# Optimization experiments

Measured on AMD Instinct MI355X. Metric: run time of the kernel, lower is better.

Reference implementation:

```python
import jax, jax.numpy as jnp
import numpy as np

NUM_PROJS = 7
BLOCK = 256       # HyperAttention block_size
SAMPLE = 256      # HyperAttention sample_size
NUM_HEADS = 16

def _hamming_perm(n):
    a = np.array([0, 1])
    for _ in range(n - 1):
        a = np.concatenate([a, a[::-1] + a.max() + 1])
    return a

_PERM = jnp.asarray(_hamming_perm(NUM_PROJS))           # [128] gray-code-ish bucket reorder
_ENC = (2 ** jnp.arange(NUM_PROJS)).astype(jnp.int32)   # [7]

def _lsh_hash(mat, proj_dir):
    # mat: [B,H,N,d], proj_dir: [d,7] -> bucket ids [B,H,N]
    bits = jnp.einsum('bhnd,dr->bhnr', mat, proj_dir) > 0
    ids = (bits * _ENC).sum(-1)
    return _PERM[ids]

def _attn_lse(q, k, v, scale, bias=None):
    s = jnp.einsum('...qd,...kd->...qk', q, k) * scale
    if bias is not None:
        s = s + bias
    lse = jax.nn.logsumexp(s, axis=-1, keepdims=True)
    o = jnp.einsum('...qk,...kd->...qd', jnp.exp(s - lse), v)
    return o, lse

def _gather(t, idx):
    # gather rows along axis 2: out[b,h,s] = t[b,h,idx[b,h,s]]
    return jnp.take_along_axis(t, idx[..., None], axis=2)

def setup_inputs():
    key = jax.random.key(0)
    ks = jax.random.split(key, 7)
    B, L, D, INNER = 2, 8192, 1024, 1024
    x = jax.random.normal(ks[0], (B, L, D), jnp.float32)
    W_qkv = jax.random.normal(ks[1], (D, 3 * INNER), jnp.float32) / np.sqrt(D)
    b_qkv = jnp.zeros((3 * INNER,), jnp.float32)
    W_proj = jax.random.normal(ks[2], (INNER, D), jnp.float32) / np.sqrt(INNER)
    b_proj = jnp.zeros((D,), jnp.float32)
    proj_dir = jax.random.normal(ks[3], (INNER // NUM_HEADS, NUM_PROJS), jnp.float32)
    sampled_set = jax.random.randint(ks[4], (B, NUM_HEADS, SAMPLE), 0, L)
    return {"x": x, "W_qkv": W_qkv, "b_qkv": b_qkv, "W_proj": W_proj,
            "b_proj": b_proj, "proj_dir": proj_dir, "sampled_set": sampled_set}

def reference(x, W_qkv, b_qkv, W_proj, b_proj, proj_dir, sampled_set):
    B, L, D = x.shape
    qkv = (x @ W_qkv + b_qkv).reshape(B, L, 3, NUM_HEADS, -1).transpose(2, 0, 3, 1, 4)
    q, k, v = qkv[0], qkv[1], qkv[2]                      # [B,H,L,dh]
    dh = q.shape[-1]
    scale = dh ** -0.5
    # 1. sortLSH: stable sort q and k rows by angular-LSH bucket id
    q_idx = jnp.argsort(_lsh_hash(q, proj_dir), axis=2, stable=True)
    k_idx = jnp.argsort(_lsh_hash(k, proj_dir), axis=2, stable=True)
    q_idx_inv = jnp.argsort(q_idx, axis=2, stable=True)   # to restore row order
    qs = _gather(q, q_idx)
    ksort = _gather(k, k_idx)
    vsort = _gather(v, k_idx)
    # block-diagonal exact attention over the sorted order (L % BLOCK == 0 here)
    nb = L // BLOCK
    ab, lb = _attn_lse(qs.reshape(B, NUM_HEADS, nb, BLOCK, dh),
                       ksort.reshape(B, NUM_HEADS, nb, BLOCK, dh),
                       vsort.reshape(B, NUM_HEADS, nb, BLOCK, dh), scale)
    attn_block = ab.reshape(B, NUM_HEADS, L, dh)
    lse_block = lb.reshape(B, NUM_HEADS, L, 1)
    # 2. residual uniformly-sampled attention, masking entries already covered by blocks
    k_sub = _gather(ksort, sampled_set)                   # [B,H,SAMPLE,dh]
    v_sub = _gather(vsort, sampled_set)
    blk_q = jnp.arange(L)[None, None, :, None] // BLOCK   # query block id (query_block_size==BLOCK)
    mask = blk_q == (sampled_set // BLOCK)[:, :, None, :]  # [B,H,L,SAMPLE]
    bias = jnp.where(mask, jnp.finfo(x.dtype).min, 0.0).astype(x.dtype)
    attn_res, lse_res = _attn_lse(qs, k_sub, v_sub, scale, bias)
    lse_res = lse_res + jnp.log(jnp.float32(L) / SAMPLE)  # importance weight n_key/sample_size
    # combine the two attentions via their log-sum-exps
    c = 1.0 / (1.0 + jnp.exp(lse_res - lse_block))
    attn = c * attn_block + (1.0 - c) * attn_res
    out = _gather(attn, q_idx_inv)                        # un-sort rows back to input order
    out = out.transpose(0, 2, 1, 3).reshape(B, L, -1)     # [B,L,inner]
    return out @ W_proj + b_proj
```

## Files before the change

### kernel.cpp

```cpp
#include <hip/hip_runtime.h>
#include <hip/hip_fp16.h>
#include <math.h>


typedef _Float16 f16x8 __attribute__((ext_vector_type(8)));
typedef _Float16 f16x4 __attribute__((ext_vector_type(4)));
typedef __fp16 fp16x2 __attribute__((ext_vector_type(2)));
typedef float f32x4 __attribute__((ext_vector_type(4)));

#define WLIST_CAP 524288
#define TAU 0.06f

__device__ __forceinline__ void gl_lds16(const void* g, void* s) {
    __builtin_amdgcn_global_load_lds(
        (const __attribute__((address_space(1))) unsigned int*)g,
        (__attribute__((address_space(3))) unsigned int*)s, 16, 0, 0);
}

__global__ __launch_bounds__(256) void fold_kernel(
    const float* __restrict__ W, const float* __restrict__ bias,
    const float* __restrict__ proj, double* __restrict__ fold,
    double* __restrict__ bfold, _Float16* __restrict__ foldh,
    float* __restrict__ bfold32)
{
    int idx = blockIdx.x * 256 + threadIdx.x;
    if (idx < 2 * 16 * 7 * 1024) {
        int task = idx / 7168;
        int rem = idx - task * 7168;
        int i = rem / 7;
        int r = rem - i * 7;
        int h = task & 15, w = task >> 4;
        double s = 0.0;
        const float* wp = W + (size_t)i * 3072 + w * 1024 + h * 64;
        for (int d = 0; d < 64; ++d)
            s += (double)wp[d] * (double)proj[d * 7 + r];
        fold[idx] = s;
        foldh[((size_t)task * 7 + r) * 1024 + i] = (_Float16)s;
    }
    if (idx < 32768)
        foldh[229376 + idx] = (_Float16)0.f;
    if (idx < 224) {
        int r = idx % 7;
        int task = idx / 7;
        int h = task & 15, w = task >> 4;
        double s = 0.0;
        for (int d = 0; d < 64; ++d)
            s += (double)bias[w * 1024 + h * 64 + d] * (double)proj[d * 7 + r];
        bfold[idx] = s;
        bfold32[idx] = (float)s;
    }
}

__global__ __launch_bounds__(256) void hashext_kernel(
    const float* __restrict__ scores, const float* __restrict__ bfold32,
    int* __restrict__ hq, int* __restrict__ hk,
    int* __restrict__ wcount, int* __restrict__ wlist)
{
    int tid = blockIdx.x * 256 + threadIdx.x;
    int row = tid >> 5, task = tid & 31;
    const float* sp = scores + (size_t)row * 256 + task * 7;
    int id = 0, fl = 0;
#pragma unroll
    for (int r = 0; r < 7; ++r) {
        float val = sp[r] + bfold32[task * 7 + r];
        if (fabsf(val) < TAU) fl = 1;
        if (val > 0.f) id |= (1 << r);
    }
    int hsh = id ^ (id >> 1);
    int w = task >> 4, h = task & 15;
    int b = row >> 13, l = row & 8191;
    (w ? hk : hq)[((size_t)(b * 16 + h) << 13) + l] = hsh;
    if (fl) {
        int slot = atomicAdd(wcount, 1);
        if (slot < WLIST_CAP) wlist[slot] = task * 16384 + row;
    }
}

__global__ __launch_bounds__(256) void refine_kernel(
    const float* __restrict__ x, const double* __restrict__ fold,
    const double* __restrict__ bfold, const int* __restrict__ wcount,
    const int* __restrict__ wlist, int* __restrict__ hq, int* __restrict__ hk)
{
    int n = *wcount;
    if (n > WLIST_CAP) n = WLIST_CAP;
    int lane = threadIdx.x & 63;
    int wid = (blockIdx.x * 256 + threadIdx.x) >> 6;
    int nw = gridDim.x * 4;
    for (int e = wid; e < n; e += nw) {
        int code = wlist[e];
        int task = code >> 14, grow = code & 16383;
        const double* f = fold + (size_t)task * 7168;
        const float* xp = x + (size_t)grow * 1024;
        double acc[7] = {0, 0, 0, 0, 0, 0, 0};
        for (int i = lane; i < 1024; i += 64) {
            double xv = (double)xp[i];
#pragma unroll
            for (int rr = 0; rr < 7; ++rr)
                acc[rr] = fma(xv, f[(size_t)i * 7 + rr], acc[rr]);
        }
        int id = 0;
#pragma unroll
        for (int rr = 0; rr < 7; ++rr) {
            double a = acc[rr];
#pragma unroll
            for (int off = 32; off > 0; off >>= 1) a += __shfl_xor(a, off, 64);
            if (a + bfold[task * 7 + rr] > 0.0) id |= (1 << rr);
        }
        if (lane == 0) {
            int hsh = id ^ (id >> 1);
            int w = task >> 4, h = task & 15;
            int b = grow >> 13, l = grow & 8191;
            (w ? hk : hq)[((size_t)(b * 16 + h) << 13) + l] = hsh;
        }
    }
}

__global__ __launch_bounds__(256) void sort_kernel(
    const int* __restrict__ hq, const int* __restrict__ hk,
    int* __restrict__ qidx, int* __restrict__ kidx,
    int* __restrict__ qrank, int* __restrict__ krank)
{
    __shared__ unsigned short cnt[128][128];
    __shared__ int tot[128];
    __shared__ int base[128];
    int blk = blockIdx.x;
    int sel = blk >> 5, bh = blk & 31;
    const int* hp = (sel ? hk : hq) + ((size_t)bh << 13);
    int* op = (sel ? kidx : qidx) + ((size_t)bh << 13);
    int* rp = (sel ? krank : qrank) + ((size_t)bh << 13);
    int t = threadIdx.x;
    for (int i = t; i < 128 * 128 / 2; i += 256) ((unsigned int*)cnt)[i] = 0u;
    __syncthreads();
    if (t < 128) {
        const int* p = hp + t * 64;
        for (int j = 0; j < 64; ++j) cnt[t][p[j]]++;
    }
    __syncthreads();
    if (t < 128) {
        int run = 0;
        for (int c = 0; c < 128; ++c) {
            int x2 = cnt[c][t];
            cnt[c][t] = (unsigned short)run;
            run += x2;
        }
        tot[t] = run;
    }
    __syncthreads();
    if (t == 0) {
        int run = 0;
        for (int v = 0; v < 128; ++v) { base[v] = run; run += tot[v]; }
    }
    __syncthreads();
    if (t < 128) {
        const int* p = hp + t * 64;
        for (int j = 0; j < 64; ++j) {
            int v = p[j];
            int c = cnt[t][v];
            cnt[t][v] = (unsigned short)(c + 1);
            int pos = base[v] + c;
            op[pos] = t * 64 + j;
            rp[t * 64 + j] = pos;
        }
    }
}

__global__ __launch_bounds__(256) void castx_kernel(
    const float* __restrict__ x, _Float16* __restrict__ xh)
{
    int i = blockIdx.x * 256 + threadIdx.x;
    float4 f = ((const float4*)x)[i];
    _Float16 h4[4] = {(_Float16)f.x, (_Float16)f.y, (_Float16)f.z, (_Float16)f.w};
    *(short4*)&xh[(size_t)i * 4] = *(short4*)h4;
}

__global__ __launch_bounds__(256) void transpose_kernel(
    const float* __restrict__ W, _Float16* __restrict__ Wt, int K, int N)
{
    __shared__ float tile[32][33];
    int bx = blockIdx.x, by = blockIdx.y;
    int tx = threadIdx.x & 31, ty = threadIdx.x >> 5;
    for (int i = ty; i < 32; i += 8)
        tile[i][tx] = W[(size_t)(by * 32 + i) * N + bx * 32 + tx];
    __syncthreads();
    for (int i = ty; i < 32; i += 8)
        Wt[(size_t)(bx * 32 + i) * K + by * 32 + tx] = (_Float16)tile[tx][i];
}

__global__ __launch_bounds__(256) void gather_samp_kernel(
    const _Float16* __restrict__ ks, const _Float16* __restrict__ vs,
    const int* __restrict__ sampled, _Float16* __restrict__ ksamp,
    _Float16* __restrict__ vsamp)
{
    int bh = blockIdx.x;
    int key = blockIdx.y * 64 + (threadIdx.x >> 2);
    int qtr = (threadIdx.x & 3) * 16;
    size_t hb = (size_t)bh << 13;
    int p = sampled[bh * 256 + key];
    size_t src = (hb + p) * 64 + qtr;
    size_t dst = ((size_t)bh * 256 + key) * 64 + qtr;
    *(f16x8*)(ksamp + dst)     = *(const f16x8*)(ks + src);
    *(f16x8*)(ksamp + dst + 8) = *(const f16x8*)(ks + src + 8);
    *(f16x8*)(vsamp + dst)     = *(const f16x8*)(vs + src);
    *(f16x8*)(vsamp + dst + 8) = *(const f16x8*)(vs + src + 8);
}

template <int MODE>
__global__ __launch_bounds__(256) void mfma_gemm(
    const _Float16* __restrict__ A, const _Float16* __restrict__ Bt,
    const float* __restrict__ bias, float* __restrict__ C, int K, int N)
{
    __shared__ __align__(16) _Float16 As[128 * 64];
    __shared__ __align__(16) _Float16 Bs[128 * 64];
    int t = threadIdx.x;
    int w = t >> 6, l = t & 63;
    int m0 = blockIdx.y * 128, n0 = blockIdx.x * 128;
    int srow = 32 * w + (l >> 3);
    int sslot = ((l & 7) ^ (l >> 3)) * 8;
    const _Float16* ga = A + (size_t)(m0 + srow) * K + sslot;
    const _Float16* gb = Bt + (size_t)(n0 + srow) * K + sslot;
    int wr = w >> 1, wc = w & 1;
    int rl = l & 15, ks = l >> 4;
    f32x4 acc[4][4];
#pragma unroll
    for (int m = 0; m < 4; ++m)
#pragma unroll
        for (int n = 0; n < 4; ++n) acc[m][n] = (f32x4){0.f, 0.f, 0.f, 0.f};
    for (int kk = 0; kk < K; kk += 64) {
        __syncthreads();
#pragma unroll
        for (int i = 0; i < 4; ++i) {
            gl_lds16(ga + (size_t)(8 * i) * K + kk, (char*)As + (32 * w + 8 * i) * 128);
            gl_lds16(gb + (size_t)(8 * i) * K + kk, (char*)Bs + (32 * w + 8 * i) * 128);
        }
        __syncthreads();
        f16x8 af[4][2], bf[4][2];
#pragma unroll
        for (int m = 0; m < 4; ++m) {
            int r = 64 * wr + 16 * m + rl;
            int sw = (r & 7) << 4;
#pragma unroll
            for (int s = 0; s < 2; ++s)
                af[m][s] = *(const f16x8*)((char*)As + r * 128 + (((s * 4 + ks) << 4) ^ sw));
        }
#pragma unroll
        for (int n = 0; n < 4; ++n) {
            int r = 64 * wc + 16 * n + rl;
            int sw = (r & 7) << 4;
#pragma unroll
            for (int s = 0; s < 2; ++s)
                bf[n][s] = *(const f16x8*)((char*)Bs + r * 128 + (((s * 4 + ks) << 4) ^ sw));
        }
#pragma unroll
        for (int m = 0; m < 4; ++m)
#pragma unroll
            for (int n = 0; n < 4; ++n) {
                acc[m][n] = __builtin_amdgcn_mfma_f32_16x16x32_f16(
                    af[m][0], bf[n][0], acc[m][n], 0, 0, 0);
                acc[m][n] = __builtin_amdgcn_mfma_f32_16x16x32_f16(
                    af[m][1], bf[n][1], acc[m][n], 0, 0, 0);
            }
    }
#pragma unroll
    for (int m = 0; m < 4; ++m)
#pragma unroll
        for (int n = 0; n < 4; ++n) {
            int gn = n0 + 64 * wc + 16 * n + rl;
            float bv = (MODE == 2) ? 0.f : bias[gn];
#pragma unroll
            for (int j = 0; j < 4; ++j) {
                int gm = m0 + 64 * wr + 16 * m + 4 * ks + j;
                C[(size_t)gm * N + gn] = acc[m][n][j] + bv;
            }
        }
}

__global__ __launch_bounds__(512) void gemm_qkv_kernel(
    const _Float16* __restrict__ Wt, const _Float16* __restrict__ xh,
    const float* __restrict__ bias, _Float16* __restrict__ Q,
    _Float16* __restrict__ Kb, _Float16* __restrict__ Vb,
    const int* __restrict__ qrank, const int* __restrict__ krank)
{
    extern __shared__ __align__(16) char smem[];
    const int K = 1024;
    int bid = blockIdx.x;
    int xcd = bid & 7, slot = bid >> 3;
    int ty = slot / 12, tx = slot - ty * 12;
    int m0 = tx * 256;
    int n0 = (xcd * 8 + ty) * 256;
    int t = threadIdx.x;
    int w = t >> 6, l = t & 63;
    int wr = w >> 2, wc = w & 3;
    int rl = l & 15, ks = l >> 4;
    int srow = t >> 3;
    int sslot = (t & 7) ^ ((t >> 3) & 7);
    const _Float16* gA = Wt + (size_t)m0 * K + sslot * 8;
    const _Float16* gB = xh + (size_t)n0 * K + sslot * 8;
    char* dstT = smem + t * 16;

    auto STAGE = [&](int buf, int op, int half, int kt) {
        const _Float16* src = op ? gB : gA;
        char* d = dstT + buf * 65536 + op * 32768 + half * 16384;
        size_t ro = (size_t)(half * 128 + srow) * K + kt * 64;
        gl_lds16(src + ro, d);
        gl_lds16(src + ro + (size_t)64 * K, d + 8192);
    };

    int fbase = m0 + 128 * wr;
    int s0 = fbase >> 10;
    int h0 = (fbase >> 6) & 15;
    int b2 = n0 >> 13;
    const int* rk = (s0 == 0) ? qrank : krank;
    _Float16* dq = (s0 == 0) ? Q : (s0 == 1 ? Kb : Vb);
    int tl = (n0 & 8191) + 64 * wc;
    int pos[2][4];
#pragma unroll
    for (int hf = 0; hf < 2; ++hf)
#pragma unroll
        for (int n = 0; n < 4; ++n)
            pos[hf][n] = rk[((size_t)(b2 * 16 + h0 + hf) << 13) + tl + 16 * n + rl];
    float4 bias4[8];
#pragma unroll
    for (int m = 0; m < 8; ++m)
        bias4[m] = *(const float4*)&bias[fbase + 16 * m + 4 * ks];

    f32x4 acc[8][4];
#pragma unroll
    for (int m = 0; m < 8; ++m)
#pragma unroll
        for (int n = 0; n < 4; ++n) acc[m][n] = (f32x4){0.f, 0.f, 0.f, 0.f};

    STAGE(0, 0, 0, 0); STAGE(0, 0, 1, 0); STAGE(0, 1, 0, 0); STAGE(0, 1, 1, 0);
    STAGE(1, 1, 0, 1); STAGE(1, 1, 1, 1);

    for (int tt = 0; tt < 16; ++tt) {
        int buf = tt & 1, obuf = buf ^ 1;
        if (tt < 15) asm volatile("s_waitcnt vmcnt(4)" ::: "memory");
        else         asm volatile("s_waitcnt vmcnt(0)" ::: "memory");
        __builtin_amdgcn_sched_barrier(0);
        __builtin_amdgcn_s_barrier();
        __builtin_amdgcn_sched_barrier(0);
        const char* Ab = smem + buf * 65536;
        const char* Bb = Ab + 32768;
        f16x8 bf[4][2], af01[2][2];
#pragma unroll
        for (int n = 0; n < 4; ++n) {
            int r = 64 * wc + 16 * n + rl;
            int sw = (r & 7) << 4;
            bf[n][0] = *(const f16x8*)(Bb + r * 128 + ((ks << 4) ^ sw));
            bf[n][1] = *(const f16x8*)(Bb + r * 128 + (((4 + ks) << 4) ^ sw));
        }
#pragma unroll
        for (int m = 0; m < 2; ++m) {
            int r = 128 * wr + 16 * m + rl;
            int sw = (r & 7) << 4;
            af01[m][0] = *(const f16x8*)(Ab + r * 128 + ((ks << 4) ^ sw));
            af01[m][1] = *(const f16x8*)(Ab + r * 128 + (((4 + ks) << 4) ^ sw));
        }
        if (tt + 1 < 16) STAGE(obuf, 0, 0, tt + 1);
        __builtin_amdgcn_s_setprio(1);
#pragma unroll
        for (int m = 0; m < 2; ++m)
#pragma unroll
            for (int n = 0; n < 4; ++n) {
                acc[m][n] = __builtin_amdgcn_mfma_f32_16x16x32_f16(
                    af01[m][0], bf[n][0], acc[m][n], 0, 0, 0);
                acc[m][n] = __builtin_amdgcn_mfma_f32_16x16x32_f16(
                    af01[m][1], bf[n][1], acc[m][n], 0, 0, 0);
            }
        __builtin_amdgcn_s_setprio(0);
        f16x8 af27[6][2];
#pragma unroll
        for (int m = 0; m < 6; ++m) {
            int r = 128 * wr + 16 * (m + 2) + rl;
            int sw = (r & 7) << 4;
            af27[m][0] = *(const f16x8*)(Ab + r * 128 + ((ks << 4) ^ sw));
            af27[m][1] = *(const f16x8*)(Ab + r * 128 + (((4 + ks) << 4) ^ sw));
        }
        if (tt + 1 < 16) STAGE(obuf, 0, 1, tt + 1);
        __builtin_amdgcn_s_setprio(1);
#pragma unroll
        for (int m = 0; m < 2; ++m)
#pragma unroll
            for (int n = 0; n < 4; ++n) {
                acc[m + 2][n] = __builtin_amdgcn_mfma_f32_16x16x32_f16(
                    af27[m][0], bf[n][0], acc[m + 2][n], 0, 0, 0);
                acc[m + 2][n] = __builtin_amdgcn_mfma_f32_16x16x32_f16(
                    af27[m][1], bf[n][1], acc[m + 2][n], 0, 0, 0);
            }
        __builtin_amdgcn_s_setprio(0);
        asm volatile("" ::: "memory");
        __builtin_amdgcn_s_barrier();
        __builtin_amdgcn_sched_barrier(0);
        if (tt + 2 < 16) STAGE(buf, 1, 0, tt + 2);
        __builtin_amdgcn_s_setprio(1);
#pragma unroll
        for (int m = 2; m < 4; ++m)
#pragma unroll
            for (int n = 0; n < 4; ++n) {
                acc[m + 2][n] = __builtin_amdgcn_mfma_f32_16x16x32_f16(
                    af27[m][0], bf[n][0], acc[m + 2][n], 0, 0, 0);
                acc[m + 2][n] = __builtin_amdgcn_mfma_f32_16x16x32_f16(
                    af27[m][1], bf[n][1], acc[m + 2][n], 0, 0, 0);
            }
        __builtin_amdgcn_s_setprio(0);
        if (tt + 2 < 16) STAGE(buf, 1, 1, tt + 2);
        __builtin_amdgcn_s_setprio(1);
#pragma unroll
        for (int m = 4; m < 6; ++m)
#pragma unroll
            for (int n = 0; n < 4; ++n) {
                acc[m + 2][n] = __builtin_amdgcn_mfma_f32_16x16x32_f16(
                    af27[m][0], bf[n][0], acc[m + 2][n], 0, 0, 0);
                acc[m + 2][n] = __builtin_amdgcn_mfma_f32_16x16x32_f16(
                    af27[m][1], bf[n][1], acc[m + 2][n], 0, 0, 0);
            }
        __builtin_amdgcn_s_setprio(0);
    }
#pragma unroll
    for (int m = 0; m < 8; ++m) {
        int hf = m >> 2;
        size_t bhb = ((size_t)(b2 * 16 + h0 + hf) << 13);
        int d = 16 * (m & 3) + 4 * ks;
#pragma unroll
        for (int n = 0; n < 4; ++n) {
            f16x4 st;
            st[0] = (_Float16)(acc[m][n][0] + bias4[m].x);
            st[1] = (_Float16)(acc[m][n][1] + bias4[m].y);
            st[2] = (_Float16)(acc[m][n][2] + bias4[m].z);
            st[3] = (_Float16)(acc[m][n][3] + bias4[m].w);
            *(f16x4*)(dq + (bhb + pos[hf][n]) * 64 + d) = st;
        }
    }
}

__global__ __launch_bounds__(256) void attn_mfma_kernel(
    const _Float16* __restrict__ qs_, const _Float16* __restrict__ ks_,
    const _Float16* __restrict__ vs_, const _Float16* __restrict__ ksamp,
    const _Float16* __restrict__ vsamp, const int* __restrict__ qidx,
    const int* __restrict__ sampled, _Float16* __restrict__ pre)
{
    __shared__ __align__(16) _Float16 Vt[2][64 * 68];
    int bid = blockIdx.x;
    int nb = (bid & 7) * 256 + (bid >> 3);
    int bh = nb >> 6, qb = (nb >> 1) & 31, half = nb & 1;
    int bb = bh >> 4, hh = bh & 15;
    size_t hb = (size_t)bh << 13;
    size_t bhs = (size_t)bh * 256;
    int t = threadIdx.x;
    int w = t >> 6, l = t & 63;
    int g = l >> 4, c16 = l & 15;
    int kg = t & 15, dg = t >> 4;
    int qw0 = qb * 256 + half * 128 + w * 32;
    const _Float16 qs = (_Float16)0.125f;

    int orig[2];
    f16x8 qf[2][2];
#pragma unroll
    for (int n = 0; n < 2; ++n) {
        int row = qw0 + 16 * n + c16;
        orig[n] = qidx[hb + row];
        const _Float16* qp = qs_ + (hb + row) * 64 + g * 8;
        qf[n][0] = *(const f16x8*)(qp);
        qf[n][1] = *(const f16x8*)(qp + 32);
#pragma unroll
        for (int j = 0; j < 8; ++j) { qf[n][0][j] *= qs; qf[n][1][j] *= qs; }
    }
    f32x4 o[4][2];
    float mr[2], lr[2];
#pragma unroll
    for (int n = 0; n < 2; ++n) {
        mr[n] = -1e30f; lr[n] = 0.f;
#pragma unroll
        for (int d2 = 0; d2 < 4; ++d2) o[d2][n] = (f32x4){0.f, 0.f, 0.f, 0.f};
    }
    const float LOG32 = 3.4657359027997265f;

    {
        const _Float16* vb = vs_ + (hb + qb * 256) * 64;
        f16x4 vr[4];
#pragma unroll
        for (int j2 = 0; j2 < 4; ++j2)
            vr[j2] = *(const f16x4*)(vb + (4 * kg + j2) * 64 + 4 * dg);
#pragma unroll
        for (int i = 0; i < 4; ++i) {
            f16x4 o4 = {vr[0][i], vr[1][i], vr[2][i], vr[3][i]};
            *(f16x4*)&Vt[0][(4 * dg + i) * 68 + 4 * kg] = o4;
        }
    }

    for (int c = 0; c < 8; ++c) {
        int cur = c & 1, nxt = cur ^ 1;
        bool samp = c >= 4;
        __syncthreads();
        const _Float16* kb = samp ? ksamp + (bhs + (size_t)(c - 4) * 64) * 64
                                  : ks_ + (hb + qb * 256 + (size_t)c * 64) * 64;
        f16x8 kf[4][2];
#pragma unroll
        for (int m = 0; m < 4; ++m) {
            const _Float16* kp = kb + (16 * m + c16) * 64 + g * 8;
            kf[m][0] = *(const f16x8*)(kp);
            kf[m][1] = *(const f16x8*)(kp + 32);
        }
        int4 spv[4];
        if (samp) {
#pragma unroll
            for (int m = 0; m < 4; ++m)
                spv[m] = *(const int4*)(sampled + bhs + (c - 4) * 64 + 16 * m + 4 * g);
        }
        f32x4 sacc[4][2];
#pragma unroll
        for (int m = 0; m < 4; ++m)
#pragma unroll
            for (int n = 0; n < 2; ++n) sacc[m][n] = (f32x4){0.f, 0.f, 0.f, 0.f};
#pragma unroll
        for (int m = 0; m < 4; ++m) {
#pragma unroll
            for (int n = 0; n < 2; ++n)
                sacc[m][n] = __builtin_amdgcn_mfma_f32_16x16x32_f16(
                    kf[m][0], qf[n][0], sacc[m][n], 0, 0, 0);
#pragma unroll
            for (int n = 0; n < 2; ++n)
                sacc[m][n] = __builtin_amdgcn_mfma_f32_16x16x32_f16(
                    kf[m][1], qf[n][1], sacc[m][n], 0, 0, 0);
        }
        f16x4 vrn[4];
        if (c < 7) {
            const _Float16* vb = (c + 1 >= 4)
                ? vsamp + (bhs + (size_t)(c - 3) * 64) * 64
                : vs_ + (hb + qb * 256 + (size_t)(c + 1) * 64) * 64;
#pragma unroll
            for (int j2 = 0; j2 < 4; ++j2)
                vrn[j2] = *(const f16x4*)(vb + (4 * kg + j2) * 64 + 4 * dg);
        }
        f16x4 av[4][4];
#pragma unroll
        for (int m = 0; m < 4; ++m)
#pragma unroll
            for (int d2 = 0; d2 < 4; ++d2)
                av[m][d2] = *(const f16x4*)&Vt[cur][(16 * d2 + c16) * 68 + 16 * m + 4 * g];
        bool msk[4][4];
#pragma unroll
        for (int m = 0; m < 4; ++m) {
            msk[m][0] = samp && ((spv[m].x >> 8) == qb);
            msk[m][1] = samp && ((spv[m].y >> 8) == qb);
            msk[m][2] = samp && ((spv[m].z >> 8) == qb);
            msk[m][3] = samp && ((spv[m].w >> 8) == qb);
        }
        float badd = samp ? LOG32 : 0.f;
#pragma unroll
        for (int n = 0; n < 2; ++n) {
            float sv[16];
#pragma unroll
            for (int m = 0; m < 4; ++m)
#pragma unroll
                for (int r = 0; r < 4; ++r)
                    sv[4 * m + r] = msk[m][r] ? -1e30f : sacc[m][n][r] + badd;
            float a0 = fmaxf(fmaxf(sv[0], sv[1]), sv[2]);
            float a1 = fmaxf(fmaxf(sv[3], sv[4]), sv[5]);
            float a2 = fmaxf(fmaxf(sv[6], sv[7]), sv[8]);
            float a3 = fmaxf(fmaxf(sv[9], sv[10]), sv[11]);
            float a4 = fmaxf(fmaxf(sv[12], sv[13]), sv[14]);
            float cm = fmaxf(fmaxf(fmaxf(a0, a1), a2), fmaxf(fmaxf(a3, a4), sv[15]));
            cm = fmaxf(cm, __shfl_xor(cm, 16, 64));
            cm = fmaxf(cm, __shfl_xor(cm, 32, 64));
            if (__any(cm > mr[n])) {
                float nm = fmaxf(mr[n], cm);
                float fq = __expf(mr[n] - nm);
                mr[n] = nm;
                lr[n] *= fq;
#pragma unroll
                for (int d2 = 0; d2 < 4; ++d2) {
                    o[d2][n][0] *= fq; o[d2][n][1] *= fq;
                    o[d2][n][2] *= fq; o[d2][n][3] *= fq;
                }
            }
            float pv16[16];
#pragma unroll
            for (int r = 0; r < 16; ++r) pv16[r] = __expf(sv[r] - mr[n]);
            float s0 = (pv16[0] + pv16[1]) + (pv16[2] + pv16[3]);
            float s1 = (pv16[4] + pv16[5]) + (pv16[6] + pv16[7]);
            float s2 = (pv16[8] + pv16[9]) + (pv16[10] + pv16[11]);
            float s3 = (pv16[12] + pv16[13]) + (pv16[14] + pv16[15]);
            float ps = (s0 + s1) + (s2 + s3);
            ps += __shfl_xor(ps, 16, 64);
            ps += __shfl_xor(ps, 32, 64);
            lr[n] += ps;
            f16x4 pb[4];
#pragma unroll
            for (int m = 0; m < 4; ++m) {
                fp16x2 c0 = __builtin_amdgcn_cvt_pkrtz(pv16[4 * m + 0], pv16[4 * m + 1]);
                fp16x2 c1 = __builtin_amdgcn_cvt_pkrtz(pv16[4 * m + 2], pv16[4 * m + 3]);
                pb[m][0] = (_Float16)c0[0]; pb[m][1] = (_Float16)c0[1];
                pb[m][2] = (_Float16)c1[0]; pb[m][3] = (_Float16)c1[1];
            }
#pragma unroll
            for (int d2 = 0; d2 < 4; ++d2)
#pragma unroll
                for (int m = 0; m < 4; ++m)
                    o[d2][n] = __builtin_amdgcn_mfma_f32_16x16x16f16(
                        av[m][d2], pb[m], o[d2][n], 0, 0, 0);
        }
        if (c < 7) {
#pragma unroll
            for (int i = 0; i < 4; ++i) {
                f16x4 o4 = {vrn[0][i], vrn[1][i], vrn[2][i], vrn[3][i]};
                *(f16x4*)&Vt[nxt][(4 * dg + i) * 68 + 4 * kg] = o4;
            }
        }
    }
#pragma unroll
    for (int n = 0; n < 2; ++n) {
        float invl = 1.f / lr[n];
        _Float16* pp = pre + ((size_t)(bb * 8192 + orig[n])) * 1024 + hh * 64;
#pragma unroll
        for (int d2 = 0; d2 < 4; ++d2) {
            f16x4 st;
            st[0] = (_Float16)(o[d2][n][0] * invl);
            st[1] = (_Float16)(o[d2][n][1] * invl);
            st[2] = (_Float16)(o[d2][n][2] * invl);
            st[3] = (_Float16)(o[d2][n][3] * invl);
            *(f16x4*)(pp + 16 * d2 + 4 * g) = st;
        }
    }
}

extern "C" void kernel_launch(void* const* d_in, const int* in_sizes, int n_in,
                              void* d_out, int out_size, void* d_ws, size_t ws_size,
                              hipStream_t stream)
{
    (void)in_sizes; (void)n_in; (void)out_size; (void)ws_size;
    const float* x     = (const float*)d_in[0];
    const float* Wqkv  = (const float*)d_in[1];
    const float* bqkv  = (const float*)d_in[2];
    const float* Wproj = (const float*)d_in[3];
    const float* bproj = (const float*)d_in[4];
    const float* proj  = (const float*)d_in[5];
    const int*   samp  = (const int*)d_in[6];
    float* out = (float*)d_out;

    char* ws = (char*)d_ws;
    size_t off = 0;
    auto take = [&](size_t bytes) {
        char* p = ws + off;
        off = (off + bytes + 255) & ~(size_t)255;
        return p;
    };
    _Float16* xh  = (_Float16*)take(33554432);
    _Float16* q   = (_Float16*)take(33554432);
    _Float16* k   = (_Float16*)take(33554432);
    _Float16* v   = (_Float16*)take(33554432);
    float* scores = (float*)take(16777216);
    _Float16* Wtq = (_Float16*)take(6291456);
    _Float16* Wtp = (_Float16*)take(2097152);
    _Float16* foldh = (_Float16*)take(524288);
    _Float16* ksamp = (_Float16*)take(1048576);
    _Float16* vsamp = (_Float16*)take(1048576);
    double* fold   = (double*)take(1835008);
    double* bfold  = (double*)take(1792);
    float* bfold32 = (float*)take(896);
    int* wcount = (int*)take(256);
    int* wlist  = (int*)take(WLIST_CAP * 4);
    int* hq    = (int*)take(1048576);
    int* hk    = (int*)take(1048576);
    int* qidx  = (int*)take(1048576);
    int* kidx  = (int*)take(1048576);
    int* qrank = (int*)take(1048576);
    int* krank = (int*)take(1048576);
    _Float16* pre = xh;

    (void)hipFuncSetAttribute((const void*)gemm_qkv_kernel,
                              hipFuncAttributeMaxDynamicSharedMemorySize, 131072);
    (void)hipMemsetAsync(wcount, 0, 4, stream);
    castx_kernel<<<dim3(16384), dim3(256), 0, stream>>>(x, xh);
    fold_kernel<<<dim3(896), dim3(256), 0, stream>>>(
        Wqkv, bqkv, proj, fold, bfold, foldh, bfold32);
    mfma_gemm<2><<<dim3(2, 128), dim3(256), 0, stream>>>(
        xh, foldh, nullptr, scores, 1024, 256);
    hashext_kernel<<<dim3(2048), dim3(256), 0, stream>>>(
        scores, bfold32, hq, hk, wcount, wlist);
    refine_kernel<<<dim3(2048), dim3(256), 0, stream>>>(
        x, fold, bfold, wcount, wlist, hq, hk);
    sort_kernel<<<dim3(64), dim3(256), 0, stream>>>(
        hq, hk, qidx, kidx, qrank, krank);
    transpose_kernel<<<dim3(96, 32), dim3(256), 0, stream>>>(Wqkv, Wtq, 1024, 3072);
    transpose_kernel<<<dim3(32, 32), dim3(256), 0, stream>>>(Wproj, Wtp, 1024, 1024);
    gemm_qkv_kernel<<<dim3(768), dim3(512), 131072, stream>>>(
        Wtq, xh, bqkv, q, k, v, qrank, krank);
    gather_samp_kernel<<<dim3(32, 4), dim3(256), 0, stream>>>(
        k, v, samp, ksamp, vsamp);
    attn_mfma_kernel<<<dim3(2048), dim3(256), 0, stream>>>(
        q, k, v, ksamp, vsamp, qidx, samp, pre);
    mfma_gemm<0><<<dim3(8, 128), dim3(256), 0, stream>>>(
        pre, Wtp, bproj, out, 1024, 1024);
}
```

Baseline: 550.6 us.

## Replace output projection GEMM with 256x256-tile pipelined MFMA kernel

Swaps the generic mfma_gemm used for the output projection for a dedicated 512-thread kernel. Each block computes a 256x256 tile, using double-buffered LDS filled by global_load_lds, XOR swizzling, and staggered prefetch of A and B halves interleaved with MFMA groups under raised priority. The larger tile raises data reuse per load, and the interleaving is meant to hide load latency. In exchange it uses 128KB of LDS, a heavy register footprint (acc[8][4] plus fragments), and only 256 blocks, which may limit occupancy and load balance.

```diff
diff --git a/kernel.cpp b/kernel.cpp
--- a/kernel.cpp
+++ b/kernel.cpp
@@ -431,6 +431,140 @@
             *(f16x4*)(dq + (bhb + pos[hf][n]) * 64 + d) = st;
         }
     }
+}
+
+__global__ __launch_bounds__(512) void gemm_out_kernel(
+    const _Float16* __restrict__ Ap, const _Float16* __restrict__ Bt,
+    const float* __restrict__ bias, float* __restrict__ C)
+{
+    extern __shared__ __align__(16) char smem[];
+    const int K = 1024;
+    int bid = blockIdx.x;
+    int m0 = (bid >> 2) * 256;
+    int n0 = (bid & 3) * 256;
+    int t = threadIdx.x;
+    int w = t >> 6, l = t & 63;
+    int wr = w >> 2, wc = w & 3;
+    int rl = l & 15, ks = l >> 4;
+    int srow = t >> 3;
+    int sslot = (t & 7) ^ ((t >> 3) & 7);
+    const _Float16* gA = Ap + (size_t)m0 * K + sslot * 8;
+    const _Float16* gB = Bt + (size_t)n0 * K + sslot * 8;
+    char* dstT = smem + t * 16;
+
+    auto STAGE = [&](int buf, int op, int half, int kt) {
+        const _Float16* src = op ? gB : gA;
+        char* d = dstT + buf * 65536 + op * 32768 + half * 16384;
+        size_t ro = (size_t)(half * 128 + srow) * K + kt * 64;
+        gl_lds16(src + ro, d);
+        gl_lds16(src + ro + (size_t)64 * K, d + 8192);
+    };
+
+    f32x4 acc[8][4];
+#pragma unroll
+    for (int m = 0; m < 8; ++m)
+#pragma unroll
+        for (int n = 0; n < 4; ++n) acc[m][n] = (f32x4){0.f, 0.f, 0.f, 0.f};
+
+    STAGE(0, 0, 0, 0); STAGE(0, 0, 1, 0); STAGE(0, 1, 0, 0); STAGE(0, 1, 1, 0);
+    STAGE(1, 1, 0, 1); STAGE(1, 1, 1, 1);
+
+    for (int tt = 0; tt < 16; ++tt) {
+        int buf = tt & 1, obuf = buf ^ 1;
+        if (tt < 15) asm volatile("s_waitcnt vmcnt(4)" ::: "memory");
+        else         asm volatile("s_waitcnt vmcnt(0)" ::: "memory");
+        __builtin_amdgcn_sched_barrier(0);
+        __builtin_amdgcn_s_barrier();
+        __builtin_amdgcn_sched_barrier(0);
+        const char* Ab = smem + buf * 65536;
+        const char* Bb = Ab + 32768;
+        f16x8 bf[4][2], af01[2][2];
+#pragma unroll
+        for (int n = 0; n < 4; ++n) {
+            int r = 64 * wc + 16 * n + rl;
+            int sw = (r & 7) << 4;
+            bf[n][0] = *(const f16x8*)(Bb + r * 128 + ((ks << 4) ^ sw));
+            bf[n][1] = *(const f16x8*)(Bb + r * 128 + (((4 + ks) << 4) ^ sw));
+        }
+#pragma unroll
+        for (int m = 0; m < 2; ++m) {
+            int r = 128 * wr + 16 * m + rl;
+            int sw = (r & 7) << 4;
+            af01[m][0] = *(const f16x8*)(Ab + r * 128 + ((ks << 4) ^ sw));
+            af01[m][1] = *(const f16x8*)(Ab + r * 128 + (((4 + ks) << 4) ^ sw));
+        }
+        if (tt + 1 < 16) STAGE(obuf, 0, 0, tt + 1);
+        __builtin_amdgcn_s_setprio(1);
+#pragma unroll
+        for (int m = 0; m < 2; ++m)
+#pragma unroll
+            for (int n = 0; n < 4; ++n) {
+                acc[m][n] = __builtin_amdgcn_mfma_f32_16x16x32_f16(
+                    af01[m][0], bf[n][0], acc[m][n], 0, 0, 0);
+                acc[m][n] = __builtin_amdgcn_mfma_f32_16x16x32_f16(
+                    af01[m][1], bf[n][1], acc[m][n], 0, 0, 0);
+            }
+        __builtin_amdgcn_s_setprio(0);
+        f16x8 af27[6][2];
+#pragma unroll
+        for (int m = 0; m < 6; ++m) {
+            int r = 128 * wr + 16 * (m + 2) + rl;
+            int sw = (r & 7) << 4;
+            af27[m][0] = *(const f16x8*)(Ab + r * 128 + ((ks << 4) ^ sw));
+            af27[m][1] = *(const f16x8*)(Ab + r * 128 + (((4 + ks) << 4) ^ sw));
+        }
+        if (tt + 1 < 16) STAGE(obuf, 0, 1, tt + 1);
+        __builtin_amdgcn_s_setprio(1);
+#pragma unroll
+        for (int m = 0; m < 2; ++m)
+#pragma unroll
+            for (int n = 0; n < 4; ++n) {
+                acc[m + 2][n] = __builtin_amdgcn_mfma_f32_16x16x32_f16(
+                    af27[m][0], bf[n][0], acc[m + 2][n], 0, 0, 0);
+                acc[m + 2][n] = __builtin_amdgcn_mfma_f32_16x16x32_f16(
+                    af27[m][1], bf[n][1], acc[m + 2][n], 0, 0, 0);
+            }
+        __builtin_amdgcn_s_setprio(0);
+        asm volatile("" ::: "memory");
+        __builtin_amdgcn_s_barrier();
+        __builtin_amdgcn_sched_barrier(0);
+        if (tt + 2 < 16) STAGE(buf, 1, 0, tt + 2);
+        __builtin_amdgcn_s_setprio(1);
+#pragma unroll
+        for (int m = 2; m < 4; ++m)
+#pragma unroll
+            for (int n = 0; n < 4; ++n) {
+                acc[m + 2][n] = __builtin_amdgcn_mfma_f32_16x16x32_f16(
+                    af27[m][0], bf[n][0], acc[m + 2][n], 0, 0, 0);
+                acc[m + 2][n] = __builtin_amdgcn_mfma_f32_16x16x32_f16(
+                    af27[m][1], bf[n][1], acc[m + 2][n], 0, 0, 0);
+            }
+        __builtin_amdgcn_s_setprio(0);
+        if (tt + 2 < 16) STAGE(buf, 1, 1, tt + 2);
+        __builtin_amdgcn_s_setprio(1);
+#pragma unroll
+        for (int m = 4; m < 6; ++m)
+#pragma unroll
+            for (int n = 0; n < 4; ++n) {
+                acc[m + 2][n] = __builtin_amdgcn_mfma_f32_16x16x32_f16(
+                    af27[m][0], bf[n][0], acc[m + 2][n], 0, 0, 0);
+                acc[m + 2][n] = __builtin_amdgcn_mfma_f32_16x16x32_f16(
+                    af27[m][1], bf[n][1], acc[m + 2][n], 0, 0, 0);
+            }
+        __builtin_amdgcn_s_setprio(0);
+    }
+#pragma unroll
+    for (int m = 0; m < 8; ++m)
+#pragma unroll
+        for (int n = 0; n < 4; ++n) {
+            int gn = n0 + 64 * wc + 16 * n + rl;
+            float bv = bias[gn];
+#pragma unroll
+            for (int j = 0; j < 4; ++j) {
+                int gm = m0 + 128 * wr + 16 * m + 4 * ks + j;
+                C[(size_t)gm * 1024 + gn] = acc[m][n][j] + bv;
+            }
+        }
 }
 
 __global__ __launch_bounds__(256) void attn_mfma_kernel(
@@ -670,6 +804,8 @@
 
     (void)hipFuncSetAttribute((const void*)gemm_qkv_kernel,
                               hipFuncAttributeMaxDynamicSharedMemorySize, 131072);
+    (void)hipFuncSetAttribute((const void*)gemm_out_kernel,
+                              hipFuncAttributeMaxDynamicSharedMemorySize, 131072);
     (void)hipMemsetAsync(wcount, 0, 4, stream);
     castx_kernel<<<dim3(16384), dim3(256), 0, stream>>>(x, xh);
     fold_kernel<<<dim3(896), dim3(256), 0, stream>>>(
@@ -690,6 +826,6 @@
         k, v, samp, ksamp, vsamp);
     attn_mfma_kernel<<<dim3(2048), dim3(256), 0, stream>>>(
         q, k, v, ksamp, vsamp, qidx, samp, pre);
-    mfma_gemm<0><<<dim3(8, 128), dim3(256), 0, stream>>>(
-        pre, Wtp, bproj, out, 1024, 1024);
-}
+    gemm_out_kernel<<<dim3(256), dim3(512), 131072, stream>>>(
+        pre, Wtp, bproj, out);
+}
```

Result: faster. 531.1 us (-3.6%).
